# Kernel optimization log

Hardware: AMD Instinct MI355X
Metric: run time of the kernel (lower is better)

## Reference

```python
import jax, jax.numpy as jnp
import numpy as np

B, S, T = 4, 1024, 1024
CTX, QIN, C, H = 1024, 1024, 1024, 16
HD = C // H  # per-head channels


def setup_inputs() -> dict:
    key = jax.random.key(0)
    ks = jax.random.split(key, 12)
    s = 0.02
    return {
        "query": jax.random.normal(ks[0], (B, S, QIN), jnp.float32),
        "key": jax.random.normal(ks[1], (B, T, CTX), jnp.float32),
        "value": jax.random.normal(ks[2], (B, T, CTX), jnp.float32),
        "mask": jax.random.randint(ks[3], (B, S, T), 0, 2).astype(bool),
        "Wq": jax.random.normal(ks[4], (C, QIN), jnp.float32) * s,
        "bq": jax.random.normal(ks[5], (C,), jnp.float32) * s,
        "Wk": jax.random.normal(ks[6], (C, CTX), jnp.float32) * s,
        "bk": jax.random.normal(ks[7], (C,), jnp.float32) * s,
        "Wv": jax.random.normal(ks[8], (C, CTX), jnp.float32) * s,
        "bv": jax.random.normal(ks[9], (C,), jnp.float32) * s,
        "Wo": jax.random.normal(ks[10], (C, C), jnp.float32) * s,
        "bo": jax.random.normal(ks[11], (C,), jnp.float32) * s,
    }


def reference(query, key, value, mask, Wq, bq, Wk, bk, Wv, bv, Wo, bo):
    b, s, _ = query.shape
    t = key.shape[1]
    c = Wq.shape[0]
    h, hd = H, c // H
    q = (query @ Wq.T + bq).reshape(b, s, h, hd)
    k = (key @ Wk.T + bk).reshape(b, t, h, hd)
    v = (value @ Wv.T + bv).reshape(b, t, h, hd)
    # [B,H,S,T] scores, scaled by 1/sqrt(head_dim)
    score = jnp.einsum('bshd,bthd->bhst', q, k) * (hd ** -0.5)
    # masked_fill_(~mask[:, None, 0:1], -inf): mask key positions via row 0
    score = jnp.where(mask[:, None, 0:1], score, -jnp.inf)
    weights = jax.nn.softmax(score, axis=-1)
    out = jnp.einsum('bhst,bthd->bshd', weights, v).reshape(b, s, c)
    out = out @ Wo.T + bo
    out = out * mask[..., 0:1].astype(out.dtype)
    return out
```

## Files before the change

### kernel.cpp

```cpp
#include <hip/hip_runtime.h>
#include <stdint.h>

#define Bb  4
#define Ss  1024
#define Tt  1024
#define Cc  1024
#define Hh  16
#define HDd 64
#define Kk  1024

typedef __bf16 bf16;
typedef __bf16 bf16x8 __attribute__((ext_vector_type(8)));
typedef float  f32x4  __attribute__((ext_vector_type(4)));
typedef __attribute__((address_space(1))) uint32_t gu32;
typedef __attribute__((address_space(3))) uint32_t lu32;

__device__ __forceinline__ void load_lds16(const bf16* g, bf16* l) {
    __builtin_amdgcn_global_load_lds((gu32*)g, (lu32*)l, 16, 0, 0);
}

#define BARRIER_LDS() do {                                    \
    asm volatile("s_waitcnt lgkmcnt(0)" ::: "memory");        \
    __builtin_amdgcn_s_barrier();                             \
} while (0)

#define BARRIER_VM() do {                                     \
    asm volatile("s_waitcnt vmcnt(0)" ::: "memory");          \
    __builtin_amdgcn_s_barrier();                             \
} while (0)

__global__ void cvt8(const float* __restrict__ s0, const float* __restrict__ s1,
                     const float* __restrict__ s2, const float* __restrict__ s3,
                     const float* __restrict__ s4, const float* __restrict__ s5,
                     const float* __restrict__ s6,
                     bf16* __restrict__ d0, bf16* __restrict__ d1,
                     bf16* __restrict__ d2, bf16* __restrict__ d3,
                     bf16* __restrict__ d4, bf16* __restrict__ d5,
                     bf16* __restrict__ d6)
{
    const float* s; bf16* d; int n;
    switch (blockIdx.y) {
        case 0: s = s0; d = d0; n = Bb * Ss * Kk; break;
        case 1: s = s1; d = d1; n = Bb * Ss * Kk; break;
        case 2: s = s2; d = d2; n = Bb * Ss * Kk; break;
        case 3: s = s3; d = d3; n = Cc * Kk; break;
        case 4: s = s4; d = d4; n = Cc * Kk; break;
        case 5: s = s5; d = d5; n = Cc * Kk; break;
        default: s = s6; d = d6; n = Cc * Kk; break;
    }
    const int i = (blockIdx.x * blockDim.x + threadIdx.x) * 8;
    if (i >= n) return;
    const float4 a = *(const float4*)(s + i);
    const float4 c = *(const float4*)(s + i + 4);
    bf16x8 o;
    o[0] = (bf16)a.x; o[1] = (bf16)a.y; o[2] = (bf16)a.z; o[3] = (bf16)a.w;
    o[4] = (bf16)c.x; o[5] = (bf16)c.y; o[6] = (bf16)c.z; o[7] = (bf16)c.w;
    *(bf16x8*)(d + i) = o;
}

__device__ __forceinline__ void mainloop_128x64_nv(
    const bf16* __restrict__ Ab, const bf16* __restrict__ Wb,
    bf16* As, bf16* Bs, f32x4 acc[4][2])
{
    const int tid  = threadIdx.x;
    const int wid  = tid >> 6;
    const int lane = tid & 63;
    const int l16  = lane & 15;
    const int quad = lane >> 4;
    const int wm   = wid >> 1;
    const int wn   = wid & 1;
    const int r8   = lane >> 3;
    const int ssw  = ((lane & 7) ^ r8) * 8;

    for (int k0 = 0; k0 < Kk; k0 += 64) {
#pragma unroll
        for (int p = 0; p < 4; p++) {
            const int rb = wid * 32 + p * 8;
            load_lds16(Ab + (size_t)(rb + r8) * Kk + k0 + ssw, As + rb * 64);
        }
#pragma unroll
        for (int p = 0; p < 2; p++) {
            const int rb = wid * 16 + p * 8;
            load_lds16(Wb + (size_t)(rb + r8) * Kk + k0 + ssw, Bs + rb * 64);
        }
        __syncthreads();
#pragma unroll
        for (int kh = 0; kh < 2; kh++) {
            bf16x8 af[4], bw[2];
#pragma unroll
            for (int i = 0; i < 4; i++)
                af[i] = *(const bf16x8*)(As + (wm * 64 + i * 16 + l16) * 64 +
                                         (((kh * 4 + quad) ^ (l16 & 7)) * 8));
#pragma unroll
            for (int j = 0; j < 2; j++)
                bw[j] = *(const bf16x8*)(Bs + (wn * 32 + j * 16 + l16) * 64 +
                                         (((kh * 4 + quad) ^ (l16 & 7)) * 8));
#pragma unroll
            for (int i = 0; i < 4; i++)
#pragma unroll
                for (int j = 0; j < 2; j++)
                    acc[i][j] = __builtin_amdgcn_mfma_f32_16x16x32_bf16(af[i], bw[j], acc[i][j], 0, 0, 0);
        }
        __syncthreads();
    }
}

__device__ __forceinline__ void mainloop_128x64_pf(
    const bf16* __restrict__ Ab, const bf16* __restrict__ Wb,
    bf16* As, bf16* Bs, f32x4 acc[4][2])
{
    const int tid  = threadIdx.x;
    const int wid  = tid >> 6;
    const int lane = tid & 63;
    const int l16  = lane & 15;
    const int quad = lane >> 4;
    const int wm   = wid >> 1;
    const int wn   = wid & 1;
    const int r8   = lane >> 3;
    const int ssw  = ((lane & 7) ^ r8) * 8;

    auto stage = [&](int k0) {
#pragma unroll
        for (int p = 0; p < 4; p++) {
            const int rb = wid * 32 + p * 8;
            load_lds16(Ab + (size_t)(rb + r8) * Kk + k0 + ssw, As + rb * 64);
        }
#pragma unroll
        for (int p = 0; p < 2; p++) {
            const int rb = wid * 16 + p * 8;
            load_lds16(Wb + (size_t)(rb + r8) * Kk + k0 + ssw, Bs + rb * 64);
        }
    };

    stage(0);
    BARRIER_VM();

    for (int k0 = 0; k0 < Kk; k0 += 64) {
        bf16x8 af[2][4], bw[2][2];
#pragma unroll
        for (int kh = 0; kh < 2; kh++) {
#pragma unroll
            for (int i = 0; i < 4; i++)
                af[kh][i] = *(const bf16x8*)(As + (wm * 64 + i * 16 + l16) * 64 +
                                             (((kh * 4 + quad) ^ (l16 & 7)) * 8));
#pragma unroll
            for (int j = 0; j < 2; j++)
                bw[kh][j] = *(const bf16x8*)(Bs + (wn * 32 + j * 16 + l16) * 64 +
                                             (((kh * 4 + quad) ^ (l16 & 7)) * 8));
        }
        BARRIER_LDS();
        if (k0 + 64 < Kk) stage(k0 + 64);
#pragma unroll
        for (int kh = 0; kh < 2; kh++)
#pragma unroll
            for (int i = 0; i < 4; i++)
#pragma unroll
                for (int j = 0; j < 2; j++)
                    acc[i][j] = __builtin_amdgcn_mfma_f32_16x16x32_bf16(af[kh][i], bw[kh][j], acc[i][j], 0, 0, 0);
        BARRIER_VM();
    }
}

__global__ __launch_bounds__(256)
void gemm_qkv(const bf16* __restrict__ Aq, const bf16* __restrict__ Ak, const bf16* __restrict__ Av,
              const bf16* __restrict__ Wq, const bf16* __restrict__ Wk, const bf16* __restrict__ Wv,
              const float* __restrict__ bq, const float* __restrict__ bk, const float* __restrict__ bv,
              const int* __restrict__ mask,
              bf16* __restrict__ Oq, bf16* __restrict__ Ok, bf16* __restrict__ Ov)
{
    __shared__ __align__(16) bf16 As[128 * 64];
    __shared__ __align__(16) bf16 Bs[64 * 64];
    __shared__ int red[256];
    __shared__ int jj[128];
    const int z = blockIdx.z;
    const bf16*  A    = (z == 0) ? Aq : (z == 1) ? Ak : Av;
    const bf16*  W    = (z == 0) ? Wq : (z == 1) ? Wk : Wv;
    const float* bias = (z == 0) ? bq : (z == 1) ? bk : bv;

    f32x4 acc[4][2];
    const f32x4 z4 = {0.f, 0.f, 0.f, 0.f};
#pragma unroll
    for (int i = 0; i < 4; i++)
#pragma unroll
        for (int j = 0; j < 2; j++) acc[i][j] = z4;

    mainloop_128x64_nv(A + (size_t)blockIdx.x * 128 * Kk,
                       W + (size_t)blockIdx.y * 64 * Kk, As, Bs, acc);

    const int tid = threadIdx.x;
    const int wid = tid >> 6, lane = tid & 63;
    const int l16 = lane & 15, quad = lane >> 4;
    const int wm = wid >> 1, wn = wid & 1;
    const int row0 = blockIdx.x * 128 + wm * 64;
    const int col0 = blockIdx.y * 64 + wn * 32;
    const int bb = (blockIdx.x * 128) >> 10;
    const int t0 = (blockIdx.x * 128) & 1023;

    if (z != 0) {
        const int* mrow = mask + (size_t)bb * Ss * Tt;
        int psum = 0;
        for (int t = tid; t < t0; t += 256) psum += (mrow[t] != 0);
        red[tid] = psum;
        __syncthreads();
        for (int off = 128; off > 0; off >>= 1) {
            if (tid < off) red[tid] += red[tid + off];
            __syncthreads();
        }
        const int base = red[0];
        if (tid < 128) jj[tid] = (mrow[t0 + tid] != 0);
        __syncthreads();
        if (tid == 0) {
            int a = base;
            for (int i = 0; i < 128; i++) { const int v = jj[i]; jj[i] = v ? a : -1; a += v; }
        }
        __syncthreads();
    }

#pragma unroll
    for (int j = 0; j < 2; j++) {
        const int col = col0 + j * 16 + l16;
        const float bj = bias[col];
        const int h = col >> 6, d = col & 63;
#pragma unroll
        for (int i = 0; i < 4; i++) {
#pragma unroll
            for (int r = 0; r < 4; r++) {
                const int local = wm * 64 + i * 16 + quad * 4 + r;
                const int row = blockIdx.x * 128 + local;
                const bf16 val = (bf16)(acc[i][j][r] + bj);
                if (z == 0) {
                    const int s = row & 1023;
                    Oq[((size_t)(bb * Hh + h) * Ss + s) * HDd + d] = val;
                } else {
                    const int jc = jj[local];
                    if (jc >= 0) {
                        if (z == 2) Ov[((size_t)((bb * Hh + h) * HDd + d)) * Tt + jc] = val;
                        else        Ok[((size_t)(bb * Hh + h) * Tt + jc) * HDd + d] = val;
                    }
                }
            }
        }
    }
}

__global__ __launch_bounds__(256)
void gemm_out(const bf16* __restrict__ A, const bf16* __restrict__ W,
              const float* __restrict__ bias, const int* __restrict__ mask,
              float* __restrict__ out)
{
    __shared__ __align__(16) bf16 As[128 * 64];
    __shared__ __align__(16) bf16 Bs[64 * 64];
    f32x4 acc[4][2];
    const f32x4 z4 = {0.f, 0.f, 0.f, 0.f};
#pragma unroll
    for (int i = 0; i < 4; i++)
#pragma unroll
        for (int j = 0; j < 2; j++) acc[i][j] = z4;

    mainloop_128x64_pf(A + (size_t)blockIdx.x * 128 * Kk,
                       W + (size_t)blockIdx.y * 64 * Kk, As, Bs, acc);

    const int tid = threadIdx.x;
    const int wid = tid >> 6, lane = tid & 63;
    const int l16 = lane & 15, quad = lane >> 4;
    const int wm = wid >> 1, wn = wid & 1;
    const int row0 = blockIdx.x * 128 + wm * 64;
    const int col0 = blockIdx.y * 64 + wn * 32;
#pragma unroll
    for (int j = 0; j < 2; j++) {
        const int col = col0 + j * 16 + l16;
        const float bj = bias[col];
#pragma unroll
        for (int i = 0; i < 4; i++) {
#pragma unroll
            for (int r = 0; r < 4; r++) {
                const int row = row0 + i * 16 + quad * 4 + r;
                const float mval = (mask[(size_t)row * Tt] != 0) ? 1.f : 0.f;
                out[(size_t)row * Cc + col] = (acc[i][j][r] + bj) * mval;
            }
        }
    }
}

__global__ __launch_bounds__(256, 2)
void attn(const bf16* __restrict__ Q, const bf16* __restrict__ Kp, const bf16* __restrict__ Vt,
          const int* __restrict__ mask, bf16* __restrict__ X)
{
    __shared__ __align__(16) bf16 Ks[64 * 64];
    __shared__ __align__(16) bf16 Vs[64 * 64];
    __shared__ __align__(16) bf16 Ps[4][32 * 72];
    __shared__ int red[256];
    const int g   = blockIdx.x;
    const int xcd = g & 7, idx = g >> 3;
    const int bh  = xcd * 8 + (idx >> 3);
    const int qblk = idx & 7;
    const int b = bh >> 4, h = bh & 15;
    const int tid = threadIdx.x, wid = tid >> 6, lane = tid & 63;
    const int l16 = lane & 15, quad = lane >> 4;
    const bf16* Qbh = Q  + (size_t)bh * Ss * HDd;
    const bf16* Kbh = Kp + (size_t)bh * Tt * HDd;
    const bf16* Vbh = Vt + (size_t)bh * HDd * Tt;
    const int*  mb  = mask + (size_t)b * Ss * Tt;
    const int q0 = qblk * 128 + wid * 32;
    bf16* Psw = &Ps[wid][0];

    int ps = 0;
    for (int t = tid; t < Tt; t += 256) ps += (mb[t] != 0);
    red[tid] = ps;
    __syncthreads();
    for (int off = 128; off > 0; off >>= 1) {
        if (tid < off) red[tid] += red[tid + off];
        __syncthreads();
    }
    const int nkb = red[0];
    const int lim = ((nkb + 127) >> 7) << 7;

    bf16x8 qf[2][2];
#pragma unroll
    for (int u = 0; u < 2; u++) {
        qf[u][0] = *(const bf16x8*)(Qbh + (size_t)(q0 + u * 16 + l16) * HDd + quad * 8);
        qf[u][1] = *(const bf16x8*)(Qbh + (size_t)(q0 + u * 16 + l16) * HDd + 32 + quad * 8);
    }

    float ls[2][4];
    f32x4 o[2][4];
    const f32x4 z4 = {0.f, 0.f, 0.f, 0.f};
#pragma unroll
    for (int u = 0; u < 2; u++)
#pragma unroll
        for (int r = 0; r < 4; r++) ls[u][r] = 0.f;
#pragma unroll
    for (int u = 0; u < 2; u++)
#pragma unroll
        for (int dblk = 0; dblk < 4; dblk++) o[u][dblk] = z4;

    const int srow = lane >> 3;
    const int schk = lane & 7;
    const int sswz = (schk ^ srow) * 8;
    const int c80 = wid * 2, c81 = wid * 2 + 1;

    const bf16* kg0 = Kbh + (size_t)(c80 * 8 + srow) * HDd + sswz;
    const bf16* kg1 = Kbh + (size_t)(c81 * 8 + srow) * HDd + sswz;
    const bf16* vg0 = Vbh + (size_t)(c80 * 8 + srow) * Tt + sswz;
    const bf16* vg1 = Vbh + (size_t)(c81 * 8 + srow) * Tt + sswz;
    bf16* kd0 = Ks + c80 * 512 + lane * 8;
    bf16* kd1 = Ks + c81 * 512 + lane * 8;
    bf16* vd0 = Vs + c80 * 512 + lane * 8;
    bf16* vd1 = Vs + c81 * 512 + lane * 8;

    bf16x8 ka0, ka1, va0, va1;
    bf16x8 kb0, kb1, vb0, vb1;

#define LOADA(KT) do { const int _kt = (KT);                          \
    ka0 = *(const bf16x8*)(kg0 + (size_t)_kt * HDd);                  \
    ka1 = *(const bf16x8*)(kg1 + (size_t)_kt * HDd);                  \
    va0 = *(const bf16x8*)(vg0 + _kt);                                \
    va1 = *(const bf16x8*)(vg1 + _kt); } while (0)
#define LOADB(KT) do { const int _kt = (KT);                          \
    kb0 = *(const bf16x8*)(kg0 + (size_t)_kt * HDd);                  \
    kb1 = *(const bf16x8*)(kg1 + (size_t)_kt * HDd);                  \
    vb0 = *(const bf16x8*)(vg0 + _kt);                                \
    vb1 = *(const bf16x8*)(vg1 + _kt); } while (0)
#define STOREA() do {                                                 \
    *(bf16x8*)kd0 = ka0; *(bf16x8*)kd1 = ka1;                         \
    *(bf16x8*)vd0 = va0; *(bf16x8*)vd1 = va1; } while (0)
#define STOREB() do {                                                 \
    *(bf16x8*)kd0 = kb0; *(bf16x8*)kd1 = kb1;                         \
    *(bf16x8*)vd0 = vb0; *(bf16x8*)vd1 = vb1; } while (0)

    auto compute = [&](int base) {
        f32x4 sc[2][4];
#pragma unroll
        for (int u = 0; u < 2; u++)
#pragma unroll
            for (int nb = 0; nb < 4; nb++) sc[u][nb] = z4;
#pragma unroll
        for (int nb = 0; nb < 4; nb++) {
            const bf16* krow = Ks + (nb * 16 + l16) * 64;
            const bf16x8 kf0 = *(const bf16x8*)(krow + ((quad       ^ (l16 & 7)) * 8));
            const bf16x8 kf1 = *(const bf16x8*)(krow + (((4 + quad) ^ (l16 & 7)) * 8));
#pragma unroll
            for (int u = 0; u < 2; u++) {
                sc[u][nb] = __builtin_amdgcn_mfma_f32_16x16x32_bf16(qf[u][0], kf0, sc[u][nb], 0, 0, 0);
                sc[u][nb] = __builtin_amdgcn_mfma_f32_16x16x32_bf16(qf[u][1], kf1, sc[u][nb], 0, 0, 0);
            }
        }

#pragma unroll
        for (int nb = 0; nb < 4; nb++) {
            const bool vv = (base + nb * 16 + l16) < nkb;
#pragma unroll
            for (int u = 0; u < 2; u++) {
#pragma unroll
                for (int r = 0; r < 4; r++) {
                    const float p = vv ? __expf(sc[u][nb][r] * 0.125f) : 0.f;
                    ls[u][r] += p;
                    Psw[(u * 16 + quad * 4 + r) * 72 + nb * 16 + l16] = (bf16)p;
                }
            }
        }

#pragma unroll
        for (int kh = 0; kh < 2; kh++) {
            const bf16x8 pf0 = *(const bf16x8*)(Psw + (l16) * 72 + kh * 32 + quad * 8);
            const bf16x8 pf1 = *(const bf16x8*)(Psw + (16 + l16) * 72 + kh * 32 + quad * 8);
#pragma unroll
            for (int dblk = 0; dblk < 4; dblk++) {
                const bf16x8 vf = *(const bf16x8*)(Vs + (dblk * 16 + l16) * 64 +
                                                   (((kh * 4 + quad) ^ (l16 & 7)) * 8));
                o[0][dblk] = __builtin_amdgcn_mfma_f32_16x16x32_bf16(pf0, vf, o[0][dblk], 0, 0, 0);
                o[1][dblk] = __builtin_amdgcn_mfma_f32_16x16x32_bf16(pf1, vf, o[1][dblk], 0, 0, 0);
            }
        }
    };

    LOADA(0);

    for (int kt = 0; kt < lim; kt += 128) {
        BARRIER_LDS();
        LOADB(kt + 64);
        STOREA();
        BARRIER_LDS();
        compute(kt);

        BARRIER_LDS();
        LOADA((kt + 128 < lim) ? (kt + 128) : (lim - 64));
        STOREB();
        BARRIER_LDS();
        compute(kt + 64);
    }
#undef LOADA
#undef LOADB
#undef STOREA
#undef STOREB

#pragma unroll
    for (int off = 1; off <= 8; off <<= 1)
#pragma unroll
        for (int u = 0; u < 2; u++)
#pragma unroll
            for (int r = 0; r < 4; r++)
                ls[u][r] += __shfl_xor(ls[u][r], off, 64);
    float inv[2][4];
#pragma unroll
    for (int u = 0; u < 2; u++)
#pragma unroll
        for (int r = 0; r < 4; r++) inv[u][r] = 1.f / ls[u][r];

#pragma unroll
    for (int u = 0; u < 2; u++) {
#pragma unroll
        for (int dblk = 0; dblk < 4; dblk++) {
#pragma unroll
            for (int r = 0; r < 4; r++) {
                const int srow_q = q0 + u * 16 + quad * 4 + r;
                const int d = dblk * 16 + l16;
                X[(size_t)(b * Ss + srow_q) * Cc + h * HDd + d] = (bf16)(o[u][dblk][r] * inv[u][r]);
            }
        }
    }
}

extern "C" void kernel_launch(void* const* d_in, const int* in_sizes, int n_in,
                              void* d_out, int out_size, void* d_ws, size_t ws_size,
                              hipStream_t stream)
{
    const float* query = (const float*)d_in[0];
    const float* key   = (const float*)d_in[1];
    const float* value = (const float*)d_in[2];
    const int*   mask  = (const int*)d_in[3];
    const float* Wq = (const float*)d_in[4];
    const float* bq = (const float*)d_in[5];
    const float* Wk = (const float*)d_in[6];
    const float* bk = (const float*)d_in[7];
    const float* Wv = (const float*)d_in[8];
    const float* bv = (const float*)d_in[9];
    const float* Wo = (const float*)d_in[10];
    const float* bo = (const float*)d_in[11];
    float* out = (float*)d_out;

    char* ws = (char*)d_ws;
    const size_t MB = 1024 * 1024;
    bf16* qb  = (bf16*)(ws + 0 * MB);
    bf16* kb  = (bf16*)(ws + 8 * MB);
    bf16* vb  = (bf16*)(ws + 16 * MB);
    bf16* wqb = (bf16*)(ws + 24 * MB);
    bf16* wkb = (bf16*)(ws + 26 * MB);
    bf16* wvb = (bf16*)(ws + 28 * MB);
    bf16* wob = (bf16*)(ws + 30 * MB);
    bf16* Qp  = (bf16*)(ws + 32 * MB);
    bf16* Kpp = (bf16*)(ws + 40 * MB);
    bf16* Vtp = (bf16*)(ws + 48 * MB);
    bf16* Xb  = (bf16*)(ws + 56 * MB);

    hipMemsetAsync(Vtp, 0, 8 * MB, stream);

    cvt8<<<dim3(2048, 7), 256, 0, stream>>>(query, key, value, Wq, Wk, Wv, Wo,
                                            qb, kb, vb, wqb, wkb, wvb, wob);
    gemm_qkv<<<dim3(32, 16, 3), 256, 0, stream>>>(qb, kb, vb, wqb, wkb, wvb,
                                                  bq, bk, bv, mask, Qp, Kpp, Vtp);
    attn<<<dim3(512), 256, 0, stream>>>(Qp, Kpp, Vtp, mask, Xb);
    gemm_out<<<dim3(32, 16), 256, 0, stream>>>(Xb, wob, bo, mask, out);
}
```

Before: 218.0 us.

## Compact masked query rows and precompute mask ranks to skip dead work

Adds a mask-scan kernel that computes prefix ranks for key columns and query rows once per batch. Conversion then scatters query, key and value rows into compacted order. The Q projection, attention and output GEMM skip tiles beyond the live-row count, and the output GEMM scatters results back through an inverse index. Output rows for masked queries come from a memset of the output buffer instead of a multiply by zero. This removes the repeated in-kernel mask reductions and roughly half of the query-side compute. In exchange it adds an extra small kernel, a full output memset and indirect scattered stores.

New measurement: 228.4 us. +4.8%, slower.

```diff
diff --git a/kernel.cpp b/kernel.cpp
--- a/kernel.cpp
+++ b/kernel.cpp
@@ -29,10 +29,47 @@
     __builtin_amdgcn_s_barrier();                             \
 } while (0)
 
+__global__ void maskscan(const int* __restrict__ mask,
+                         int* __restrict__ rankK, int* __restrict__ nkK,
+                         int* __restrict__ rankQ, int* __restrict__ nkQ,
+                         int* __restrict__ invQ)
+{
+    const int b = blockIdx.x;
+    const int kind = blockIdx.y;
+    const int tid = threadIdx.x;
+    const int* mb = mask + (size_t)b * Ss * Tt;
+    __shared__ int part[256];
+    int v[4]; int s = 0;
+#pragma unroll
+    for (int u = 0; u < 4; u++) {
+        const int idx = tid * 4 + u;
+        v[u] = kind ? (mb[(size_t)idx * Tt] != 0) : (mb[idx] != 0);
+        s += v[u];
+    }
+    part[tid] = s; __syncthreads();
+    for (int off = 1; off < 256; off <<= 1) {
+        const int t_ = (tid >= off) ? part[tid - off] : 0;
+        __syncthreads();
+        part[tid] += t_;
+        __syncthreads();
+    }
+    int a = part[tid] - s;
+#pragma unroll
+    for (int u = 0; u < 4; u++) {
+        const int idx = tid * 4 + u;
+        const int j = v[u] ? a : -1;
+        if (kind) { rankQ[b * Tt + idx] = j; if (j >= 0) invQ[b * Tt + j] = idx; }
+        else      { rankK[b * Tt + idx] = j; }
+        a += v[u];
+    }
+    if (tid == 255) { if (kind) nkQ[b] = a; else nkK[b] = a; }
+}
+
 __global__ void cvt8(const float* __restrict__ s0, const float* __restrict__ s1,
                      const float* __restrict__ s2, const float* __restrict__ s3,
                      const float* __restrict__ s4, const float* __restrict__ s5,
                      const float* __restrict__ s6,
+                     const int* __restrict__ rankK, const int* __restrict__ rankQ,
                      bf16* __restrict__ d0, bf16* __restrict__ d1,
                      bf16* __restrict__ d2, bf16* __restrict__ d3,
                      bf16* __restrict__ d4, bf16* __restrict__ d5,
@@ -50,12 +87,20 @@
     }
     const int i = (blockIdx.x * blockDim.x + threadIdx.x) * 8;
     if (i >= n) return;
+    int dsti = i;
+    if (blockIdx.y <= 2) {
+        const int row = i >> 10;
+        const int b = row >> 10, t = row & 1023;
+        const int j = (blockIdx.y == 0) ? rankQ[b * Tt + t] : rankK[b * Tt + t];
+        if (j < 0) return;
+        dsti = (((b << 10) + j) << 10) + (i & 1023);
+    }
     const float4 a = *(const float4*)(s + i);
     const float4 c = *(const float4*)(s + i + 4);
     bf16x8 o;
     o[0] = (bf16)a.x; o[1] = (bf16)a.y; o[2] = (bf16)a.z; o[3] = (bf16)a.w;
     o[4] = (bf16)c.x; o[5] = (bf16)c.y; o[6] = (bf16)c.z; o[7] = (bf16)c.w;
-    *(bf16x8*)(d + i) = o;
+    *(bf16x8*)(d + dsti) = o;
 }
 
 __device__ __forceinline__ void mainloop_128x64_nv(
@@ -165,14 +210,17 @@
 void gemm_qkv(const bf16* __restrict__ Aq, const bf16* __restrict__ Ak, const bf16* __restrict__ Av,
               const bf16* __restrict__ Wq, const bf16* __restrict__ Wk, const bf16* __restrict__ Wv,
               const float* __restrict__ bq, const float* __restrict__ bk, const float* __restrict__ bv,
-              const int* __restrict__ mask,
+              const int* __restrict__ nkK, const int* __restrict__ nkQ,
               bf16* __restrict__ Oq, bf16* __restrict__ Ok, bf16* __restrict__ Ov)
 {
     __shared__ __align__(16) bf16 As[128 * 64];
     __shared__ __align__(16) bf16 Bs[64 * 64];
-    __shared__ int red[256];
-    __shared__ int jj[128];
     const int z = blockIdx.z;
+    const int bb = blockIdx.x >> 3;
+    const int t0 = (blockIdx.x & 7) * 128;
+    const int nlim = (z == 0) ? nkQ[bb] : nkK[bb];
+    if (t0 >= nlim) return;
+
     const bf16*  A    = (z == 0) ? Aq : (z == 1) ? Ak : Av;
     const bf16*  W    = (z == 0) ? Wq : (z == 1) ? Wk : Wv;
     const float* bias = (z == 0) ? bq : (z == 1) ? bk : bv;
@@ -191,30 +239,7 @@
     const int wid = tid >> 6, lane = tid & 63;
     const int l16 = lane & 15, quad = lane >> 4;
     const int wm = wid >> 1, wn = wid & 1;
-    const int row0 = blockIdx.x * 128 + wm * 64;
     const int col0 = blockIdx.y * 64 + wn * 32;
-    const int bb = (blockIdx.x * 128) >> 10;
-    const int t0 = (blockIdx.x * 128) & 1023;
-
-    if (z != 0) {
-        const int* mrow = mask + (size_t)bb * Ss * Tt;
-        int psum = 0;
-        for (int t = tid; t < t0; t += 256) psum += (mrow[t] != 0);
-        red[tid] = psum;
-        __syncthreads();
-        for (int off = 128; off > 0; off >>= 1) {
-            if (tid < off) red[tid] += red[tid + off];
-            __syncthreads();
-        }
-        const int base = red[0];
-        if (tid < 128) jj[tid] = (mrow[t0 + tid] != 0);
-        __syncthreads();
-        if (tid == 0) {
-            int a = base;
-            for (int i = 0; i < 128; i++) { const int v = jj[i]; jj[i] = v ? a : -1; a += v; }
-        }
-        __syncthreads();
-    }
 
 #pragma unroll
     for (int j = 0; j < 2; j++) {
@@ -225,18 +250,12 @@
         for (int i = 0; i < 4; i++) {
 #pragma unroll
             for (int r = 0; r < 4; r++) {
-                const int local = wm * 64 + i * 16 + quad * 4 + r;
-                const int row = blockIdx.x * 128 + local;
-                const bf16 val = (bf16)(acc[i][j][r] + bj);
-                if (z == 0) {
-                    const int s = row & 1023;
-                    Oq[((size_t)(bb * Hh + h) * Ss + s) * HDd + d] = val;
-                } else {
-                    const int jc = jj[local];
-                    if (jc >= 0) {
-                        if (z == 2) Ov[((size_t)((bb * Hh + h) * HDd + d)) * Tt + jc] = val;
-                        else        Ok[((size_t)(bb * Hh + h) * Tt + jc) * HDd + d] = val;
-                    }
+                const int jrow = t0 + wm * 64 + i * 16 + quad * 4 + r;
+                if (jrow < nlim) {
+                    const bf16 val = (bf16)(acc[i][j][r] + bj);
+                    if (z == 0)      Oq[((size_t)(bb * Hh + h) * Ss + jrow) * HDd + d] = val;
+                    else if (z == 1) Ok[((size_t)(bb * Hh + h) * Tt + jrow) * HDd + d] = val;
+                    else             Ov[((size_t)((bb * Hh + h) * HDd + d)) * Tt + jrow] = val;
                 }
             }
         }
@@ -245,9 +264,15 @@
 
 __global__ __launch_bounds__(256)
 void gemm_out(const bf16* __restrict__ A, const bf16* __restrict__ W,
-              const float* __restrict__ bias, const int* __restrict__ mask,
+              const float* __restrict__ bias,
+              const int* __restrict__ nkQ, const int* __restrict__ invQ,
               float* __restrict__ out)
 {
+    const int bb = blockIdx.x >> 3;
+    const int t0 = (blockIdx.x & 7) * 128;
+    const int nq = nkQ[bb];
+    if (t0 >= nq) return;
+
     __shared__ __align__(16) bf16 As[128 * 64];
     __shared__ __align__(16) bf16 Bs[64 * 64];
     f32x4 acc[4][2];
@@ -264,7 +289,6 @@
     const int wid = tid >> 6, lane = tid & 63;
     const int l16 = lane & 15, quad = lane >> 4;
     const int wm = wid >> 1, wn = wid & 1;
-    const int row0 = blockIdx.x * 128 + wm * 64;
     const int col0 = blockIdx.y * 64 + wn * 32;
 #pragma unroll
     for (int j = 0; j < 2; j++) {
@@ -274,9 +298,11 @@
         for (int i = 0; i < 4; i++) {
 #pragma unroll
             for (int r = 0; r < 4; r++) {
-                const int row = row0 + i * 16 + quad * 4 + r;
-                const float mval = (mask[(size_t)row * Tt] != 0) ? 1.f : 0.f;
-                out[(size_t)row * Cc + col] = (acc[i][j][r] + bj) * mval;
+                const int jrow = t0 + wm * 64 + i * 16 + quad * 4 + r;
+                if (jrow < nq) {
+                    const int s = invQ[bb * Tt + jrow];
+                    out[((size_t)bb * Ss + s) * Cc + col] = acc[i][j][r] + bj;
+                }
             }
         }
     }
@@ -284,36 +310,28 @@
 
 __global__ __launch_bounds__(256, 2)
 void attn(const bf16* __restrict__ Q, const bf16* __restrict__ Kp, const bf16* __restrict__ Vt,
-          const int* __restrict__ mask, bf16* __restrict__ X)
+          const int* __restrict__ nkK, const int* __restrict__ nkQ, bf16* __restrict__ X)
 {
     __shared__ __align__(16) bf16 Ks[64 * 64];
     __shared__ __align__(16) bf16 Vs[64 * 64];
     __shared__ __align__(16) bf16 Ps[4][32 * 72];
-    __shared__ int red[256];
     const int g   = blockIdx.x;
     const int xcd = g & 7, idx = g >> 3;
     const int bh  = xcd * 8 + (idx >> 3);
     const int qblk = idx & 7;
     const int b = bh >> 4, h = bh & 15;
+    const int nq  = nkQ[b];
+    if (qblk * 128 >= nq) return;
+    const int nkb = nkK[b];
+    const int lim = ((nkb + 127) >> 7) << 7;
+
     const int tid = threadIdx.x, wid = tid >> 6, lane = tid & 63;
     const int l16 = lane & 15, quad = lane >> 4;
     const bf16* Qbh = Q  + (size_t)bh * Ss * HDd;
     const bf16* Kbh = Kp + (size_t)bh * Tt * HDd;
     const bf16* Vbh = Vt + (size_t)bh * HDd * Tt;
-    const int*  mb  = mask + (size_t)b * Ss * Tt;
     const int q0 = qblk * 128 + wid * 32;
     bf16* Psw = &Ps[wid][0];
-
-    int ps = 0;
-    for (int t = tid; t < Tt; t += 256) ps += (mb[t] != 0);
-    red[tid] = ps;
-    __syncthreads();
-    for (int off = 128; off > 0; off >>= 1) {
-        if (tid < off) red[tid] += red[tid + off];
-        __syncthreads();
-    }
-    const int nkb = red[0];
-    const int lim = ((nkb + 127) >> 7) << 7;
 
     bf16x8 qf[2][2];
 #pragma unroll
@@ -454,8 +472,10 @@
 #pragma unroll
             for (int r = 0; r < 4; r++) {
                 const int srow_q = q0 + u * 16 + quad * 4 + r;
-                const int d = dblk * 16 + l16;
-                X[(size_t)(b * Ss + srow_q) * Cc + h * HDd + d] = (bf16)(o[u][dblk][r] * inv[u][r]);
+                if (srow_q < nq) {
+                    const int d = dblk * 16 + l16;
+                    X[(size_t)(b * Ss + srow_q) * Cc + h * HDd + d] = (bf16)(o[u][dblk][r] * inv[u][r]);
+                }
             }
         }
     }
@@ -493,12 +513,23 @@
     bf16* Vtp = (bf16*)(ws + 48 * MB);
     bf16* Xb  = (bf16*)(ws + 56 * MB);
 
+    char* intb = ws + 64 * MB - 64 * 1024;
+    int* rankK = (int*)(intb);
+    int* rankQ = (int*)(intb + 16 * 1024);
+    int* invQ  = (int*)(intb + 32 * 1024);
+    int* nkK   = (int*)(intb + 48 * 1024);
+    int* nkQ   = (int*)(intb + 48 * 1024 + 256);
+
     hipMemsetAsync(Vtp, 0, 8 * MB, stream);
-
+    hipMemsetAsync(out, 0, (size_t)out_size, stream);
+
+    maskscan<<<dim3(4, 2), 256, 0, stream>>>(mask, rankK, nkK, rankQ, nkQ, invQ);
     cvt8<<<dim3(2048, 7), 256, 0, stream>>>(query, key, value, Wq, Wk, Wv, Wo,
+                                            rankK, rankQ,
                                             qb, kb, vb, wqb, wkb, wvb, wob);
     gemm_qkv<<<dim3(32, 16, 3), 256, 0, stream>>>(qb, kb, vb, wqb, wkb, wvb,
-                                                  bq, bk, bv, mask, Qp, Kpp, Vtp);
-    attn<<<dim3(512), 256, 0, stream>>>(Qp, Kpp, Vtp, mask, Xb);
-    gemm_out<<<dim3(32, 16), 256, 0, stream>>>(Xb, wob, bo, mask, out);
-}
+                                                  bq, bk, bv, nkK, nkQ,
+                                                  Qp, Kpp, Vtp);
+    attn<<<dim3(512), 256, 0, stream>>>(Qp, Kpp, Vtp, nkK, nkQ, Xb);
+    gemm_out<<<dim3(32, 16), 256, 0, stream>>>(Xb, wob, bo, nkQ, invQ, out);
+}
```
